# Performance work log

Measured on AMD Instinct MI355X. Metric: run time of the kernel, lower is better.

Reference implementation:

```python
import jax, jax.numpy as jnp
import numpy as np
from jax.ops import segment_sum, segment_max

N, E, B, F, CG = 20000, 320000, 64, 256, 92
NL, NP = 4, 3  # transformer conv layers, ppe layers
SQ = float(np.sqrt(F))


def setup_inputs() -> dict:
    ks = iter(jax.random.split(jax.random.key(0), 64))
    p = lambda *s: jax.random.normal(next(ks), s, jnp.float32) * 0.02
    return {
        "x": jax.random.uniform(next(ks), (N, CG), jnp.float32, 0.0, 10.0),
        "edge_index": jax.random.randint(next(ks), (2, E), 0, N, dtype=jnp.int32),
        "edge_attr": jax.random.normal(next(ks), (E, 3), jnp.float32),
        "batch": jnp.sort(jax.random.randint(next(ks), (N,), 0, B, dtype=jnp.int32)),
        "num_osda": jax.random.uniform(next(ks), (B,), jnp.float32, 1.0, 4.0),
        "ae_W1": p(F, CG), "ae_b1": p(F), "ae_W2": p(F, F), "ae_b2": p(F),
        "ee_W": p(F, F), "ee_b": p(F),
        "pe_W": p(F, CG), "pe_b": p(F),
        "Wq": p(NL, F, F), "bq": p(NL, F), "Wk": p(NL, F, F), "bk": p(NL, F),
        "Wv": p(NL, F, F), "bv": p(NL, F), "We": p(NL, F, F), "be": p(NL, F),
        "Ws": p(NL, F, F), "bs": p(NL, F),
        "pW1": p(NP, 2 * F, F), "pb1": p(NP, 2 * F),
        "pW2": p(NP, F, F), "pb2": p(NP, F),
        "pW3": p(NP, F, F), "pb3": p(NP, F),
        "pg": jnp.ones((NP, F), jnp.float32), "pbeta": jnp.zeros((NP, F), jnp.float32),
        "fc_W": p(F, F), "fc_b": p(F), "out_W": p(1, F), "out_b": p(1),
    }


def _forward(x, edge_index, edge_attr, batch, num_osda, ae_W1, ae_b1, ae_W2, ae_b2,
             ee_W, ee_b, pe_W, pe_b, Wq, bq, Wk, bk, Wv, bv, We, be, Ws, bs,
             pW1, pb1, pW2, pb2, pW3, pb3, pg, pbeta, fc_W, fc_b, out_W, out_b):
    src, dst = edge_index[0], edge_index[1]
    # atom embedding on floor(x): Lin -> SiLU -> Lin
    h = jax.nn.silu(jnp.floor(x) @ ae_W1.T + ae_b1) @ ae_W2.T + ae_b2   # [N,F]
    # ppe embedding on frac(x)*1000
    ppe = ((x - jnp.trunc(x)) * 1000.0) @ pe_W.T + pe_b                 # [N,F]
    # edge embedding: scalar -1/||edge_attr|| -> RBF(vmin=-6,vmax=0,bins=256) -> Lin -> SiLU
    d = -1.0 / jnp.linalg.norm(edge_attr, axis=1)                       # [E]
    centers = jnp.linspace(-6.0, 0.0, F)
    gamma = 1.0 / (6.0 / (F - 1))  # 1/mean(diff(centers))
    rbf = jnp.exp(-gamma * (d[:, None] - centers) ** 2)                 # [E,F]
    ef = jax.nn.silu(rbf @ ee_W.T + ee_b)                               # [E,F]

    def conv(h, i):
        # graph transformer conv (heads=1): softmax over incoming edges per node
        q = h @ Wq[i].T + bq[i]
        k = h @ Wk[i].T + bk[i]
        v = h @ Wv[i].T + bv[i]
        e = ef @ We[i].T + be[i]
        kj = k[src] + e                                                 # [E,F]
        vj = v[src] + e                                                 # [E,F]
        s = jnp.sum(q[dst] * kj, axis=-1) / SQ                          # [E]
        m = segment_max(s, dst, num_segments=N)
        ex = jnp.exp(s - m[dst])
        den = segment_sum(ex, dst, num_segments=N)
        alpha = ex / den[dst]
        agg = segment_sum(alpha[:, None] * vj, dst, num_segments=N)     # [N,F]
        return agg + h @ Ws[i].T + bs[i]                                # root/skip

    def ppe_conv(h, adj, i):
        adj = adj + h
        bn = adj * pg[i] + pbeta[i]  # eval-mode BatchNorm1d (running mean 0, var 1)
        a2 = bn @ pW1[i].T + pb1[i]                                     # [N,2F]
        x1 = a2[:, :F] @ pW2[i].T + pb2[i]
        x2 = jax.nn.gelu(a2[:, F:], approximate=False)  # dropout = identity (eval)
        return (x1 * x2) @ pW3[i].T + pb3[i] + h, adj

    for i in range(NP):
        h = conv(h, i)
        h, ppe = ppe_conv(h, ppe, i)
    h = conv(h, NL - 1)

    # scatter-mean pooling over graphs
    cnt = jnp.maximum(segment_sum(jnp.ones((N,), h.dtype), batch, num_segments=B), 1.0)
    tot = segment_sum(h, batch, num_segments=B) / cnt[:, None]          # [B,F]
    crystal = tot + jax.nn.silu(tot @ fc_W.T + fc_b)
    out = crystal @ out_W.T + out_b                                     # [B,1]
    return jnp.squeeze(out, -1) / num_osda                             # [B]


def reference(x, edge_index, edge_attr, batch, num_osda, ae_W1, ae_b1, ae_W2, ae_b2,
              ee_W, ee_b, pe_W, pe_b, Wq, bq, Wk, bk, Wv, bv, We, be, Ws, bs,
              pW1, pb1, pW2, pb2, pW3, pb3, pg, pbeta, fc_W, fc_b, out_W, out_b):
    return _forward(x, edge_index, edge_attr, batch, num_osda, ae_W1, ae_b1, ae_W2, ae_b2,
                    ee_W, ee_b, pe_W, pe_b, Wq, bq, Wk, bk, Wv, bv, We, be, Ws, bs,
                    pW1, pb1, pW2, pb2, pW3, pb3, pg, pbeta, fc_W, fc_b, out_W, out_b)
```

## Files before the change

### kernel.cpp

```cpp
#include <hip/hip_runtime.h>
#include <cstdint>
#include <cstddef>


#define DEVFN static __device__ __forceinline__

DEVFN float siluf(float x) { return x / (1.f + expf(-x)); }

DEVFN unsigned short f2bf(float x) {
    union { float f; unsigned u; } v; v.f = x;
    return (unsigned short)((v.u + 0x7FFFu + ((v.u >> 16) & 1u)) >> 16);
}
DEVFN float bf2f(unsigned short h) {
    union { unsigned u; float f; } v; v.u = ((unsigned)h) << 16;
    return v.f;
}

typedef __attribute__((ext_vector_type(8))) short bf16x8;
typedef __attribute__((ext_vector_type(4))) float f32x4;

template <int ACT>
__launch_bounds__(256) __global__
void gemm_sw(const float* __restrict__ A, int lda,
             const short* __restrict__ Whi, const short* __restrict__ Wlo, int Kp,
             const float* __restrict__ bias,
             const float* __restrict__ res, int ldr,
             float* __restrict__ C, int ldc,
             int M, int K, int OUT)
{
    constexpr int LDP = 40;
    __shared__ short AsH[128 * LDP];
    __shared__ short AsL[128 * LDP];
    __shared__ short WsH[128 * LDP];
    __shared__ short WsL[128 * LDP];
    const int tid = threadIdx.x;
    const int bm = blockIdx.x * 128;
    const int bn = blockIdx.y * 128;
    const int w = tid >> 6, lane = tid & 63;
    const int wm = (w >> 1) * 64, wn = (w & 1) * 64;
    const int lr = lane & 15, lc = lane >> 4;

    f32x4 acc[4][4];
#pragma unroll
    for (int i = 0; i < 4; ++i)
#pragma unroll
        for (int j = 0; j < 4; ++j) acc[i][j] = (f32x4){0.f, 0.f, 0.f, 0.f};

    const int srow = tid & 127;
    const int scol0 = (tid >> 7) * 16;

    for (int k0 = 0; k0 < K; k0 += 32) {
        {
            int gm = bm + srow;
            const float* ap = A + (size_t)gm * lda + k0 + scol0;
            short sh[16], sl[16];
#pragma unroll
            for (int q = 0; q < 4; ++q) {
                int c = k0 + scol0 + q * 4;
                float4 vv = {0.f, 0.f, 0.f, 0.f};
                if (gm < M) {
                    if (c + 3 < K) {
                        vv = *reinterpret_cast<const float4*>(ap + q * 4);
                    } else {
                        if (c < K)     vv.x = ap[q * 4 + 0];
                        if (c + 1 < K) vv.y = ap[q * 4 + 1];
                        if (c + 2 < K) vv.z = ap[q * 4 + 2];
                        if (c + 3 < K) vv.w = ap[q * 4 + 3];
                    }
                }
                float e[4] = {vv.x, vv.y, vv.z, vv.w};
#pragma unroll
                for (int t = 0; t < 4; ++t) {
                    unsigned short hi = f2bf(e[t]);
                    sh[q * 4 + t] = (short)hi;
                    sl[q * 4 + t] = (short)f2bf(e[t] - bf2f(hi));
                }
            }
            *reinterpret_cast<bf16x8*>(&AsH[srow * LDP + scol0])     = *reinterpret_cast<bf16x8*>(&sh[0]);
            *reinterpret_cast<bf16x8*>(&AsH[srow * LDP + scol0 + 8]) = *reinterpret_cast<bf16x8*>(&sh[8]);
            *reinterpret_cast<bf16x8*>(&AsL[srow * LDP + scol0])     = *reinterpret_cast<bf16x8*>(&sl[0]);
            *reinterpret_cast<bf16x8*>(&AsL[srow * LDP + scol0 + 8]) = *reinterpret_cast<bf16x8*>(&sl[8]);
        }
        {
            int go = bn + srow;
            if (go < OUT) {
                const short* wh = Whi + (size_t)go * Kp + k0 + scol0;
                const short* wl = Wlo + (size_t)go * Kp + k0 + scol0;
                *reinterpret_cast<bf16x8*>(&WsH[srow * LDP + scol0])     = *reinterpret_cast<const bf16x8*>(wh);
                *reinterpret_cast<bf16x8*>(&WsH[srow * LDP + scol0 + 8]) = *reinterpret_cast<const bf16x8*>(wh + 8);
                *reinterpret_cast<bf16x8*>(&WsL[srow * LDP + scol0])     = *reinterpret_cast<const bf16x8*>(wl);
                *reinterpret_cast<bf16x8*>(&WsL[srow * LDP + scol0 + 8]) = *reinterpret_cast<const bf16x8*>(wl + 8);
            } else {
                bf16x8 z = {0, 0, 0, 0, 0, 0, 0, 0};
                *reinterpret_cast<bf16x8*>(&WsH[srow * LDP + scol0])     = z;
                *reinterpret_cast<bf16x8*>(&WsH[srow * LDP + scol0 + 8]) = z;
                *reinterpret_cast<bf16x8*>(&WsL[srow * LDP + scol0])     = z;
                *reinterpret_cast<bf16x8*>(&WsL[srow * LDP + scol0 + 8]) = z;
            }
        }
        __syncthreads();

        bf16x8 afh[4], afl[4], bfh[4], bfl[4];
#pragma unroll
        for (int f = 0; f < 4; ++f) {
            afh[f] = *reinterpret_cast<const bf16x8*>(&AsH[(wm + f * 16 + lr) * LDP + lc * 8]);
            afl[f] = *reinterpret_cast<const bf16x8*>(&AsL[(wm + f * 16 + lr) * LDP + lc * 8]);
            bfh[f] = *reinterpret_cast<const bf16x8*>(&WsH[(wn + f * 16 + lr) * LDP + lc * 8]);
            bfl[f] = *reinterpret_cast<const bf16x8*>(&WsL[(wn + f * 16 + lr) * LDP + lc * 8]);
        }
#pragma unroll
        for (int i = 0; i < 4; ++i)
#pragma unroll
            for (int j = 0; j < 4; ++j) {
                acc[i][j] = __builtin_amdgcn_mfma_f32_16x16x32_bf16(afh[i], bfh[j], acc[i][j], 0, 0, 0);
                acc[i][j] = __builtin_amdgcn_mfma_f32_16x16x32_bf16(afh[i], bfl[j], acc[i][j], 0, 0, 0);
                acc[i][j] = __builtin_amdgcn_mfma_f32_16x16x32_bf16(afl[i], bfh[j], acc[i][j], 0, 0, 0);
            }
        __syncthreads();
    }

#pragma unroll
    for (int i = 0; i < 4; ++i) {
#pragma unroll
        for (int j = 0; j < 4; ++j) {
            int col = bn + wn + j * 16 + lr;
            if (col >= OUT) continue;
            float bv = bias ? bias[col] : 0.f;
#pragma unroll
            for (int r = 0; r < 4; ++r) {
                int m = bm + wm + i * 16 + lc * 4 + r;
                if (m < M) {
                    float v = acc[i][j][r] + bv;
                    if (ACT == 1) v = siluf(v);
                    if (res) v += res[(size_t)m * ldr + col];
                    C[(size_t)m * ldc + col] = v;
                }
            }
        }
    }
}

template <int BM, int BN, int TM, int TN, int ACT>
__launch_bounds__(256) __global__
void gemm_nt(const float* __restrict__ A, int lda,
             const float* __restrict__ W,
             const float* __restrict__ bias,
             const float* __restrict__ res, int ldr,
             float* __restrict__ C, int ldc,
             int M, int K, int OUT)
{
    constexpr int BK = 16;
    __shared__ alignas(16) float As[BK][BM];
    __shared__ alignas(16) float Bs[BK][BN];
    const int tid = threadIdx.x;
    const int bm = blockIdx.x * BM;
    const int bn = blockIdx.y * BN;
    const int tr = (tid >> 4) * TM;
    const int tc = (tid & 15) * TN;

    float acc[TM][TN];
#pragma unroll
    for (int i = 0; i < TM; ++i)
#pragma unroll
        for (int j = 0; j < TN; ++j) acc[i][j] = 0.f;

    for (int k0 = 0; k0 < K; k0 += BK) {
#pragma unroll
        for (int it = 0; it < BM / 64; ++it) {
            int idx = tid + it * 256;
            int m = idx >> 2, kq = idx & 3;
            int gm = bm + m, gk = k0 + kq * 4;
            float t[4] = {0.f, 0.f, 0.f, 0.f};
            if (gm < M) {
#pragma unroll
                for (int j = 0; j < 4; ++j)
                    if (gk + j < K) t[j] = A[(size_t)gm * lda + gk + j];
            }
            As[kq * 4 + 0][m] = t[0];
            As[kq * 4 + 1][m] = t[1];
            As[kq * 4 + 2][m] = t[2];
            As[kq * 4 + 3][m] = t[3];
        }
#pragma unroll
        for (int it = 0; it < BN / 64; ++it) {
            int idx = tid + it * 256;
            int o = idx >> 2, kq = idx & 3;
            int go = bn + o, gk = k0 + kq * 4;
            float t[4] = {0.f, 0.f, 0.f, 0.f};
            if (go < OUT) {
#pragma unroll
                for (int j = 0; j < 4; ++j)
                    if (gk + j < K) t[j] = W[(size_t)go * K + gk + j];
            }
            Bs[kq * 4 + 0][o] = t[0];
            Bs[kq * 4 + 1][o] = t[1];
            Bs[kq * 4 + 2][o] = t[2];
            Bs[kq * 4 + 3][o] = t[3];
        }
        __syncthreads();
#pragma unroll
        for (int kk = 0; kk < BK; ++kk) {
            float a[TM], b[TN];
#pragma unroll
            for (int p = 0; p < TM; ++p) a[p] = As[kk][tr + p];
#pragma unroll
            for (int p = 0; p < TN; ++p) b[p] = Bs[kk][tc + p];
#pragma unroll
            for (int i = 0; i < TM; ++i)
#pragma unroll
                for (int j = 0; j < TN; ++j) acc[i][j] += a[i] * b[j];
        }
        __syncthreads();
    }

#pragma unroll
    for (int i = 0; i < TM; ++i) {
        int m = bm + tr + i;
        if (m >= M) continue;
#pragma unroll
        for (int j = 0; j < TN; ++j) {
            int o = bn + tc + j;
            if (o >= OUT) continue;
            float v = acc[i][j];
            if (bias) v += bias[o];
            if (ACT == 1) v = siluf(v);
            if (res) v += res[(size_t)m * ldr + o];
            C[(size_t)m * ldc + o] = v;
        }
    }
}

__global__ void split_w_k(const float* __restrict__ src, short* __restrict__ dhi,
                          short* __restrict__ dlo, int OUT, int K, int Kp)
{
    int idx = blockIdx.x * blockDim.x + threadIdx.x;
    if (idx >= OUT * Kp) return;
    int row = idx / Kp, col = idx - row * Kp;
    float v = (col < K) ? src[(size_t)row * K + col] : 0.f;
    unsigned short hi = f2bf(v);
    dhi[idx] = (short)hi;
    dlo[idx] = (short)f2bf(v - bf2f(hi));
}

__global__ void stack_qkvs_w_k(const float* __restrict__ Wq, const float* __restrict__ Wk,
                               const float* __restrict__ Wv, const float* __restrict__ Ws,
                               short* __restrict__ dhi, short* __restrict__ dlo, int total)
{
    int idx = blockIdx.x * blockDim.x + threadIdx.x;
    if (idx >= total) return;
    int col = idx & 255;
    int row = (idx >> 8) & 1023;
    int layer = idx >> 18;
    int s2 = row >> 8;
    const float* s = (s2 == 0) ? Wq : ((s2 == 1) ? Wk : ((s2 == 2) ? Wv : Ws));
    float v = s[(size_t)layer * 65536 + (size_t)(row & 255) * 256 + col];
    unsigned short hi = f2bf(v);
    dhi[idx] = (short)hi;
    dlo[idx] = (short)f2bf(v - bf2f(hi));
}

__global__ void stack_qkvs_b_k(const float* __restrict__ bq, const float* __restrict__ bk,
                               const float* __restrict__ bv, const float* __restrict__ bs,
                               float* __restrict__ dst, int total)
{
    int idx = blockIdx.x * blockDim.x + threadIdx.x;
    if (idx >= total) return;
    int r = idx & 1023, layer = idx >> 10;
    int s2 = r >> 8;
    const float* s = (s2 == 0) ? bq : ((s2 == 1) ? bk : ((s2 == 2) ? bv : bs));
    dst[idx] = s[layer * 256 + (r & 255)];
}

__global__ void node_prep_k(const float* __restrict__ x, float* __restrict__ fx,
                            float* __restrict__ px, int n)
{
    int i = blockIdx.x * blockDim.x + threadIdx.x;
    if (i < n) {
        float v = x[i];
        fx[i] = floorf(v);
        px[i] = (v - truncf(v)) * 1000.f;
    }
}

__global__ void table_rbf_k(float* __restrict__ out, int T, float dmin, float step)
{
    int idx = blockIdx.x * blockDim.x + threadIdx.x;
    if (idx >= T * 64) return;
    int t = idx >> 6, j4 = (idx & 63) * 4;
    float dv = dmin + step * (float)t;
    float r[4];
#pragma unroll
    for (int j = 0; j < 4; ++j) {
        float c = -6.f + 6.f * (float)(j4 + j) * (1.f / 255.f);
        float u = dv - c;
        r[j] = expf(-42.5f * u * u);
    }
    float4 v = {r[0], r[1], r[2], r[3]};
    *reinterpret_cast<float4*>(out + (size_t)t * 256 + j4) = v;
}

__global__ void edge_prep_k(const float* __restrict__ ea, int* __restrict__ i0,
                            float* __restrict__ fr, int E, float dmin, float invstep, int T)
{
    int i = blockIdx.x * blockDim.x + threadIdx.x;
    if (i < E) {
        float a = ea[(size_t)i * 3], b = ea[(size_t)i * 3 + 1], c = ea[(size_t)i * 3 + 2];
        float d = -1.f / sqrtf(a * a + b * b + c * c);
        float u = (d - dmin) * invstep;
        u = fminf(fmaxf(u, 0.f), (float)(T - 1) - 1e-3f);
        int t0 = (int)u;
        i0[i] = t0;
        fr[i] = u - (float)t0;
    }
}

__global__ void ppe_prep_k(float* __restrict__ ppe, const float* __restrict__ h,
                           const float* __restrict__ pg, const float* __restrict__ pbeta,
                           float* __restrict__ bn, int n)
{
    int i = blockIdx.x * blockDim.x + threadIdx.x;
    if (i < n) {
        float adj = ppe[i] + h[i];
        ppe[i] = adj;
        int f = i & 255;
        bn[i] = adj * pg[f] + pbeta[f];
    }
}

__global__ void gate_k(const float* __restrict__ x1, const float* __restrict__ a2,
                       float* __restrict__ g, int n)
{
    int i = blockIdx.x * blockDim.x + threadIdx.x;
    if (i < n) {
        int m = i >> 8, f = i & 255;
        float x2 = a2[(size_t)m * 512 + 256 + f];
        float ge = 0.5f * x2 * (1.f + erff(x2 * 0.70710678118654752f));
        g[i] = x1[i] * ge;
    }
}

__global__ void hist_k(const int* __restrict__ dst, int* __restrict__ deg, int E)
{
    int i = blockIdx.x * blockDim.x + threadIdx.x;
    if (i < E) atomicAdd(&deg[dst[i]], 1);
}

__global__ void scan_k(const int* __restrict__ deg, int* __restrict__ off, int n)
{
    __shared__ int buf[1024];
    __shared__ int carry;
    const int t = threadIdx.x;
    if (t == 0) carry = 0;
    __syncthreads();
    for (int base = 0; base < n; base += 1024) {
        int i = base + t;
        int v = (i < n) ? deg[i] : 0;
        buf[t] = v;
        __syncthreads();
        for (int s = 1; s < 1024; s <<= 1) {
            int add = (t >= s) ? buf[t - s] : 0;
            __syncthreads();
            buf[t] += add;
            __syncthreads();
        }
        if (i < n) off[i] = carry + buf[t] - v;
        __syncthreads();
        if (t == 0) carry += buf[1023];
        __syncthreads();
    }
    if (t == 0) off[n] = carry;
}

__global__ void copy_int_k(const int* __restrict__ a, int* __restrict__ b, int n)
{
    int i = blockIdx.x * blockDim.x + threadIdx.x;
    if (i < n) b[i] = a[i];
}

__global__ void scatter_k(const int* __restrict__ dst, int* __restrict__ cursor,
                          int* __restrict__ esort, int E)
{
    int i = blockIdx.x * blockDim.x + threadIdx.x;
    if (i < E) {
        int p = atomicAdd(&cursor[dst[i]], 1);
        esort[p] = i;
    }
}

__launch_bounds__(256) __global__
void attn_fused_k(const float* __restrict__ qkvs, const float* __restrict__ etab,
                  const int* __restrict__ ei0, const float* __restrict__ efr,
                  const int* __restrict__ src, const int* __restrict__ esort,
                  const int* __restrict__ off, float* __restrict__ hn, int Nn)
{
    int node = blockIdx.x * 4 + (threadIdx.x >> 6);
    if (node >= Nn) return;
    int lane = threadIdx.x & 63;
    int lo = off[node], hi = off[node + 1];

    const float* qrow = qkvs + (size_t)node * 1024;
    float4 qv = *reinterpret_cast<const float4*>(qrow + lane * 4);
    float4 sk = *reinterpret_cast<const float4*>(qrow + 768 + lane * 4);

    float m = -3.4e38f, den = 0.f;
    float ax = 0.f, ay = 0.f, az = 0.f, aw = 0.f;

    for (int jj = lo; jj < hi; ++jj) {
        int eid = esort[jj];
        int sp = src[eid];
        int t0 = ei0[eid];
        float f = efr[eid];
        const float* srow = qkvs + (size_t)sp * 1024;
        float4 kv = *reinterpret_cast<const float4*>(srow + 256 + lane * 4);
        float4 e0 = *reinterpret_cast<const float4*>(etab + (size_t)t0 * 256 + lane * 4);
        float4 e1 = *reinterpret_cast<const float4*>(etab + (size_t)(t0 + 1) * 256 + lane * 4);
        float ex0 = e0.x + f * (e1.x - e0.x);
        float ex1 = e0.y + f * (e1.y - e0.y);
        float ex2 = e0.z + f * (e1.z - e0.z);
        float ex3 = e0.w + f * (e1.w - e0.w);
        float p = qv.x * (kv.x + ex0) + qv.y * (kv.y + ex1) +
                  qv.z * (kv.z + ex2) + qv.w * (kv.w + ex3);
#pragma unroll
        for (int s = 32; s; s >>= 1) p += __shfl_xor(p, s, 64);
        p *= 0.0625f;
        float4 vv = *reinterpret_cast<const float4*>(srow + 512 + lane * 4);
        float vx0 = vv.x + ex0, vx1 = vv.y + ex1, vx2 = vv.z + ex2, vx3 = vv.w + ex3;
        if (p > m) {
            float sc = expf(m - p);
            den = den * sc + 1.f;
            ax = ax * sc + vx0;
            ay = ay * sc + vx1;
            az = az * sc + vx2;
            aw = aw * sc + vx3;
            m = p;
        } else {
            float wgt = expf(p - m);
            den += wgt;
            ax += wgt * vx0;
            ay += wgt * vx1;
            az += wgt * vx2;
            aw += wgt * vx3;
        }
    }
    float inv = (hi > lo) ? 1.f / den : 0.f;
    float4 o = {sk.x + ax * inv, sk.y + ay * inv, sk.z + az * inv, sk.w + aw * inv};
    *reinterpret_cast<float4*>(hn + (size_t)node * 256 + lane * 4) = o;
}

__launch_bounds__(256) __global__
void pool_mean_k(const float* __restrict__ h, const int* __restrict__ batch,
                 float* __restrict__ tot, int Nn)
{
    int g = blockIdx.x;
    __shared__ int sl, sh;
    if (threadIdx.x == 0) {
        int lo = 0, hi = Nn;
        while (lo < hi) { int mid = (lo + hi) >> 1; if (batch[mid] < g) lo = mid + 1; else hi = mid; }
        sl = lo;
        lo = 0; hi = Nn;
        while (lo < hi) { int mid = (lo + hi) >> 1; if (batch[mid] < g + 1) lo = mid + 1; else hi = mid; }
        sh = lo;
    }
    __syncthreads();
    float acc = 0.f;
    for (int n = sl; n < sh; ++n) acc += h[(size_t)n * 256 + threadIdx.x];
    float c = (float)(sh - sl);
    if (c < 1.f) c = 1.f;
    tot[(size_t)g * 256 + threadIdx.x] = acc / c;
}

__launch_bounds__(256) __global__
void out_k(const float* __restrict__ crystal, const float* __restrict__ oW,
           const float* __restrict__ ob, const float* __restrict__ nosda,
           float* __restrict__ out, int Bn)
{
    int b = blockIdx.x;
    __shared__ float red[256];
    float p = crystal[(size_t)b * 256 + threadIdx.x] * oW[threadIdx.x];
    red[threadIdx.x] = p;
    __syncthreads();
    for (int s = 128; s; s >>= 1) {
        if (threadIdx.x < s) red[threadIdx.x] += red[threadIdx.x + s];
        __syncthreads();
    }
    if (threadIdx.x == 0) out[b] = (red[0] + ob[0]) / nosda[b];
}

extern "C" void kernel_launch(void* const* d_in, const int* in_sizes, int n_in,
                              void* d_out, int out_size, void* d_ws, size_t ws_size,
                              hipStream_t stream)
{
    const float* x     = (const float*)d_in[0];
    const int*   ei    = (const int*)d_in[1];
    const float* ea    = (const float*)d_in[2];
    const int*   batch = (const int*)d_in[3];
    const float* nosda = (const float*)d_in[4];
    const float* ae_W1 = (const float*)d_in[5];
    const float* ae_b1 = (const float*)d_in[6];
    const float* ae_W2 = (const float*)d_in[7];
    const float* ae_b2 = (const float*)d_in[8];
    const float* ee_W  = (const float*)d_in[9];
    const float* ee_b  = (const float*)d_in[10];
    const float* pe_W  = (const float*)d_in[11];
    const float* pe_b  = (const float*)d_in[12];
    const float* Wq    = (const float*)d_in[13];
    const float* bq    = (const float*)d_in[14];
    const float* Wk    = (const float*)d_in[15];
    const float* bk    = (const float*)d_in[16];
    const float* Wv    = (const float*)d_in[17];
    const float* bv    = (const float*)d_in[18];
    const float* We    = (const float*)d_in[19];
    const float* be    = (const float*)d_in[20];
    const float* Ws    = (const float*)d_in[21];
    const float* bs    = (const float*)d_in[22];
    const float* pW1   = (const float*)d_in[23];
    const float* pb1   = (const float*)d_in[24];
    const float* pW2   = (const float*)d_in[25];
    const float* pb2   = (const float*)d_in[26];
    const float* pW3   = (const float*)d_in[27];
    const float* pb3   = (const float*)d_in[28];
    const float* pg    = (const float*)d_in[29];
    const float* pbeta = (const float*)d_in[30];
    const float* fc_W  = (const float*)d_in[31];
    const float* fc_b  = (const float*)d_in[32];
    const float* out_W = (const float*)d_in[33];
    const float* out_b = (const float*)d_in[34];

    const int CG = 92, F = 256;
    const int N = in_sizes[0] / CG;
    const int E = in_sizes[1] / 2;
    const int B = in_sizes[4];
    const int T = 4096;
    const float DMIN = -8.f, DMAX = 0.f;
    const float STEP = (DMAX - DMIN) / (float)(T - 1);
    const int* src  = ei;
    const int* dstp = ei + E;

    float* w = (float*)d_ws;
    auto take = [&](size_t n) { float* p = w; w += n; return p; };
    auto takeS = [&](size_t nshorts) { short* p = (short*)w; w += (nshorts + 1) / 2; return p; };
    const size_t NF = (size_t)N * F;
    const size_t NCG = (size_t)N * CG;
    float* hb0  = take(NF);
    float* hb1  = take(NF);
    float* ppeb = take(NF);
    float* s1   = take(NF);
    float* arena = take((size_t)N * 1024);
    float* qkvs = arena;
    float* a2b  = arena;
    float* s2b  = arena + 2 * NF;
    float* s3   = arena + 3 * NF;
    float* fx   = arena;
    float* px   = arena + NCG;
    float* rbft = arena + 2 * NCG;
    float* eft  = arena + 2 * NCG + (size_t)T * F;
    float* etab = take((size_t)4 * T * F);
    float* efr  = take(E);
    float* totb = take((size_t)B * F);
    float* cryb = take((size_t)B * F);
    float* bstk = take(4 * 1024);
    short* qwHi = takeS((size_t)4 * 1024 * 256);
    short* qwLo = takeS((size_t)4 * 1024 * 256);
    short* eeHi = takeS((size_t)256 * 256);
    short* eeLo = takeS((size_t)256 * 256);
    short* weHi = takeS((size_t)4 * 256 * 256);
    short* weLo = takeS((size_t)4 * 256 * 256);
    short* a1Hi = takeS((size_t)256 * 96);
    short* a1Lo = takeS((size_t)256 * 96);
    short* a2Hi = takeS((size_t)256 * 256);
    short* a2Lo = takeS((size_t)256 * 256);
    short* peHi = takeS((size_t)256 * 96);
    short* peLo = takeS((size_t)256 * 96);
    short* p1Hi = takeS((size_t)3 * 512 * 256);
    short* p1Lo = takeS((size_t)3 * 512 * 256);
    short* p2Hi = takeS((size_t)3 * 256 * 256);
    short* p2Lo = takeS((size_t)3 * 256 * 256);
    short* p3Hi = takeS((size_t)3 * 256 * 256);
    short* p3Lo = takeS((size_t)3 * 256 * 256);
    int* ei0    = (int*)w; w += E;
    int* deg    = (int*)w; w += N;
    int* offb   = (int*)w; w += (N + 1);
    int* curb   = (int*)w; w += N;
    int* esort  = (int*)w; w += E;
    size_t need = (size_t)((char*)w - (char*)d_ws);
    if (need > ws_size) return;
    (void)n_in; (void)out_size;

    dim3 blk(256);
    auto g1 = [](int n) { return dim3((n + 255) / 256); };

    auto gsw = [&](const float* A, int lda, const short* Whi, const short* Wlo, int Kp,
                   const float* bias, const float* res, int ldr, float* C, int ldc,
                   int M, int K, int OUT, int act) {
        dim3 grid((M + 127) / 128, (OUT + 127) / 128);
        if (act)
            gemm_sw<1><<<grid, blk, 0, stream>>>(A, lda, Whi, Wlo, Kp, bias, res, ldr, C, ldc, M, K, OUT);
        else
            gemm_sw<0><<<grid, blk, 0, stream>>>(A, lda, Whi, Wlo, Kp, bias, res, ldr, C, ldc, M, K, OUT);
    };

    node_prep_k<<<g1(N * CG), blk, 0, stream>>>(x, fx, px, N * CG);
    edge_prep_k<<<g1(E), blk, 0, stream>>>(ea, ei0, efr, E, DMIN, 1.f / STEP, T);
    table_rbf_k<<<g1(T * 64), blk, 0, stream>>>(rbft, T, DMIN, STEP);

    stack_qkvs_w_k<<<g1(4 * 1024 * 256), blk, 0, stream>>>(Wq, Wk, Wv, Ws, qwHi, qwLo, 4 * 1024 * 256);
    stack_qkvs_b_k<<<g1(4 * 1024), blk, 0, stream>>>(bq, bk, bv, bs, bstk, 4 * 1024);
    split_w_k<<<g1(256 * 256), blk, 0, stream>>>(ee_W, eeHi, eeLo, 256, 256, 256);
    split_w_k<<<g1(4 * 256 * 256), blk, 0, stream>>>(We, weHi, weLo, 1024, 256, 256);
    split_w_k<<<g1(256 * 96), blk, 0, stream>>>(ae_W1, a1Hi, a1Lo, 256, 92, 96);
    split_w_k<<<g1(256 * 256), blk, 0, stream>>>(ae_W2, a2Hi, a2Lo, 256, 256, 256);
    split_w_k<<<g1(256 * 96), blk, 0, stream>>>(pe_W, peHi, peLo, 256, 92, 96);
    split_w_k<<<g1(3 * 512 * 256), blk, 0, stream>>>(pW1, p1Hi, p1Lo, 1536, 256, 256);
    split_w_k<<<g1(3 * 256 * 256), blk, 0, stream>>>(pW2, p2Hi, p2Lo, 768, 256, 256);
    split_w_k<<<g1(3 * 256 * 256), blk, 0, stream>>>(pW3, p3Hi, p3Lo, 768, 256, 256);

    gsw(rbft, F, eeHi, eeLo, 256, ee_b, nullptr, 0, eft, F, T, F, F, 1);
    for (int i = 0; i < 4; ++i)
        gsw(eft, F, weHi + (size_t)i * 65536, weLo + (size_t)i * 65536, 256,
            be + (size_t)i * F, nullptr, 0, etab + (size_t)i * T * F, F, T, F, F, 0);

    gsw(fx, CG, a1Hi, a1Lo, 96, ae_b1, nullptr, 0, s1, F, N, CG, F, 1);
    gsw(s1, F, a2Hi, a2Lo, 256, ae_b2, nullptr, 0, hb0, F, N, F, F, 0);
    gsw(px, CG, peHi, peLo, 96, pe_b, nullptr, 0, ppeb, F, N, CG, F, 0);

    hipMemsetAsync(deg, 0, (size_t)N * sizeof(int), stream);
    hist_k<<<g1(E), blk, 0, stream>>>(dstp, deg, E);
    scan_k<<<1, 1024, 0, stream>>>(deg, offb, N);
    copy_int_k<<<g1(N), blk, 0, stream>>>(offb, curb, N);
    scatter_k<<<g1(E), blk, 0, stream>>>(dstp, curb, esort, E);

    float* h  = hb0;
    float* hn = hb1;
    for (int i = 0; i < 4; ++i) {
        gsw(h, F, qwHi + (size_t)i * 1024 * 256, qwLo + (size_t)i * 1024 * 256, 256,
            bstk + (size_t)i * 1024, nullptr, 0, qkvs, 1024, N, F, 1024, 0);

        attn_fused_k<<<dim3((N + 3) / 4), blk, 0, stream>>>(
            qkvs, etab + (size_t)i * T * F, ei0, efr, src, esort, offb, hn, N);
        { float* t = h; h = hn; hn = t; }

        if (i < 3) {
            ppe_prep_k<<<g1(N * F), blk, 0, stream>>>(ppeb, h, pg + (size_t)i * F, pbeta + (size_t)i * F, s1, N * F);
            gsw(s1, F, p1Hi + (size_t)i * 512 * 256, p1Lo + (size_t)i * 512 * 256, 256,
                pb1 + (size_t)i * 2 * F, nullptr, 0, a2b, 2 * F, N, F, 2 * F, 0);
            gsw(a2b, 2 * F, p2Hi + (size_t)i * 65536, p2Lo + (size_t)i * 65536, 256,
                pb2 + (size_t)i * F, nullptr, 0, s2b, F, N, F, F, 0);
            gate_k<<<g1(N * F), blk, 0, stream>>>(s2b, a2b, s3, N * F);
            gsw(s3, F, p3Hi + (size_t)i * 65536, p3Lo + (size_t)i * 65536, 256,
                pb3 + (size_t)i * F, h, F, hn, F, N, F, F, 0);
            { float* t = h; h = hn; hn = t; }
        }
    }

    pool_mean_k<<<dim3(B), blk, 0, stream>>>(h, batch, totb, N);
    {
        dim3 grid((B + 63) / 64, (F + 63) / 64);
        gemm_nt<64, 64, 4, 4, 1><<<grid, blk, 0, stream>>>(totb, F, fc_W, fc_b, totb, F, cryb, F, B, F, F);
    }
    out_k<<<dim3(B), blk, 0, stream>>>(cryb, out_W, out_b, nosda, (float*)d_out, B);
}
```

Baseline: 1.834 ms.

## Feed GEMMs pre-split bf16 hi/lo planes produced by upstream kernel epilogues

The split-bf16 GEMM now reads activations that are already stored as bf16 hi/lo planes, instead of loading fp32 and splitting in its inner loop. Producers do the split in their epilogues: elementwise prep kernels, the RBF table, the gate kernel, and GEMMs through new output modes (planes only, fp32 plus planes, and a PPE mode that separates the two halves). The PPE first GEMM also writes its second half contiguously, so the gate kernel reads it without striding. This removes repeated conversion ALU work and the ragged K-edge load paths from every GEMM tile. The cost is extra plane stores in some epilogues and more buffer aliasing in the arena.

```diff
diff --git a/kernel.cpp b/kernel.cpp
--- a/kernel.cpp
+++ b/kernel.cpp
@@ -19,14 +19,19 @@
 typedef __attribute__((ext_vector_type(8))) short bf16x8;
 typedef __attribute__((ext_vector_type(4))) float f32x4;
 
-template <int ACT>
+#define O_F32    0
+#define O_F32P   1
+#define O_PPE1   4
+#define O_PLANES 5
+
+template <int ACT, int OMODE>
 __launch_bounds__(256) __global__
-void gemm_sw(const float* __restrict__ A, int lda,
-             const short* __restrict__ Whi, const short* __restrict__ Wlo, int Kp,
-             const float* __restrict__ bias,
-             const float* __restrict__ res, int ldr,
-             float* __restrict__ C, int ldc,
-             int M, int K, int OUT)
+void gemm_spp(const short* __restrict__ Ahi, const short* __restrict__ Alo, int lda,
+              const short* __restrict__ Whi, const short* __restrict__ Wlo, int ldw,
+              const float* __restrict__ bias,
+              const float* __restrict__ res, int ldr,
+              float* __restrict__ C, short* __restrict__ P1, short* __restrict__ P2,
+              int ldc, int M, int OUT, int K)
 {
     constexpr int LDP = 40;
     __shared__ short AsH[128 * LDP];
@@ -52,40 +57,26 @@
     for (int k0 = 0; k0 < K; k0 += 32) {
         {
             int gm = bm + srow;
-            const float* ap = A + (size_t)gm * lda + k0 + scol0;
-            short sh[16], sl[16];
-#pragma unroll
-            for (int q = 0; q < 4; ++q) {
-                int c = k0 + scol0 + q * 4;
-                float4 vv = {0.f, 0.f, 0.f, 0.f};
-                if (gm < M) {
-                    if (c + 3 < K) {
-                        vv = *reinterpret_cast<const float4*>(ap + q * 4);
-                    } else {
-                        if (c < K)     vv.x = ap[q * 4 + 0];
-                        if (c + 1 < K) vv.y = ap[q * 4 + 1];
-                        if (c + 2 < K) vv.z = ap[q * 4 + 2];
-                        if (c + 3 < K) vv.w = ap[q * 4 + 3];
-                    }
-                }
-                float e[4] = {vv.x, vv.y, vv.z, vv.w};
-#pragma unroll
-                for (int t = 0; t < 4; ++t) {
-                    unsigned short hi = f2bf(e[t]);
-                    sh[q * 4 + t] = (short)hi;
-                    sl[q * 4 + t] = (short)f2bf(e[t] - bf2f(hi));
-                }
-            }
-            *reinterpret_cast<bf16x8*>(&AsH[srow * LDP + scol0])     = *reinterpret_cast<bf16x8*>(&sh[0]);
-            *reinterpret_cast<bf16x8*>(&AsH[srow * LDP + scol0 + 8]) = *reinterpret_cast<bf16x8*>(&sh[8]);
-            *reinterpret_cast<bf16x8*>(&AsL[srow * LDP + scol0])     = *reinterpret_cast<bf16x8*>(&sl[0]);
-            *reinterpret_cast<bf16x8*>(&AsL[srow * LDP + scol0 + 8]) = *reinterpret_cast<bf16x8*>(&sl[8]);
+            if (gm < M) {
+                const short* ah = Ahi + (size_t)gm * lda + k0 + scol0;
+                const short* al = Alo + (size_t)gm * lda + k0 + scol0;
+                *reinterpret_cast<bf16x8*>(&AsH[srow * LDP + scol0])     = *reinterpret_cast<const bf16x8*>(ah);
+                *reinterpret_cast<bf16x8*>(&AsH[srow * LDP + scol0 + 8]) = *reinterpret_cast<const bf16x8*>(ah + 8);
+                *reinterpret_cast<bf16x8*>(&AsL[srow * LDP + scol0])     = *reinterpret_cast<const bf16x8*>(al);
+                *reinterpret_cast<bf16x8*>(&AsL[srow * LDP + scol0 + 8]) = *reinterpret_cast<const bf16x8*>(al + 8);
+            } else {
+                bf16x8 z = {0, 0, 0, 0, 0, 0, 0, 0};
+                *reinterpret_cast<bf16x8*>(&AsH[srow * LDP + scol0])     = z;
+                *reinterpret_cast<bf16x8*>(&AsH[srow * LDP + scol0 + 8]) = z;
+                *reinterpret_cast<bf16x8*>(&AsL[srow * LDP + scol0])     = z;
+                *reinterpret_cast<bf16x8*>(&AsL[srow * LDP + scol0 + 8]) = z;
+            }
         }
         {
             int go = bn + srow;
             if (go < OUT) {
-                const short* wh = Whi + (size_t)go * Kp + k0 + scol0;
-                const short* wl = Wlo + (size_t)go * Kp + k0 + scol0;
+                const short* wh = Whi + (size_t)go * ldw + k0 + scol0;
+                const short* wl = Wlo + (size_t)go * ldw + k0 + scol0;
                 *reinterpret_cast<bf16x8*>(&WsH[srow * LDP + scol0])     = *reinterpret_cast<const bf16x8*>(wh);
                 *reinterpret_cast<bf16x8*>(&WsH[srow * LDP + scol0 + 8]) = *reinterpret_cast<const bf16x8*>(wh + 8);
                 *reinterpret_cast<bf16x8*>(&WsL[srow * LDP + scol0])     = *reinterpret_cast<const bf16x8*>(wl);
@@ -129,11 +120,30 @@
 #pragma unroll
             for (int r = 0; r < 4; ++r) {
                 int m = bm + wm + i * 16 + lc * 4 + r;
-                if (m < M) {
-                    float v = acc[i][j][r] + bv;
-                    if (ACT == 1) v = siluf(v);
+                if (m >= M) continue;
+                float v = acc[i][j][r] + bv;
+                if (ACT == 1) v = siluf(v);
+                if (OMODE == O_F32) {
                     if (res) v += res[(size_t)m * ldr + col];
                     C[(size_t)m * ldc + col] = v;
+                } else if (OMODE == O_F32P) {
+                    if (res) v += res[(size_t)m * ldr + col];
+                    C[(size_t)m * ldc + col] = v;
+                    unsigned short hi = f2bf(v);
+                    P1[(size_t)m * ldc + col] = (short)hi;
+                    P2[(size_t)m * ldc + col] = (short)f2bf(v - bf2f(hi));
+                } else if (OMODE == O_PPE1) {
+                    if (col < 256) {
+                        unsigned short hi = f2bf(v);
+                        P1[(size_t)m * 256 + col] = (short)hi;
+                        P2[(size_t)m * 256 + col] = (short)f2bf(v - bf2f(hi));
+                    } else {
+                        C[(size_t)m * 256 + (col - 256)] = v;
+                    }
+                } else {
+                    unsigned short hi = f2bf(v);
+                    P1[(size_t)m * ldc + col] = (short)hi;
+                    P2[(size_t)m * ldc + col] = (short)f2bf(v - bf2f(hi));
                 }
             }
         }
@@ -271,32 +281,44 @@
     dst[idx] = s[layer * 256 + (r & 255)];
 }
 
-__global__ void node_prep_k(const float* __restrict__ x, float* __restrict__ fx,
-                            float* __restrict__ px, int n)
-{
-    int i = blockIdx.x * blockDim.x + threadIdx.x;
-    if (i < n) {
-        float v = x[i];
-        fx[i] = floorf(v);
-        px[i] = (v - truncf(v)) * 1000.f;
-    }
-}
-
-__global__ void table_rbf_k(float* __restrict__ out, int T, float dmin, float step)
+__global__ void node_prep_k(const float* __restrict__ x,
+                            short* __restrict__ fxHi, short* __restrict__ fxLo,
+                            short* __restrict__ pxHi, short* __restrict__ pxLo, int n96)
+{
+    int idx = blockIdx.x * blockDim.x + threadIdx.x;
+    if (idx >= n96) return;
+    int n = idx / 96, c = idx - n * 96;
+    float fv = 0.f, pv = 0.f;
+    if (c < 92) {
+        float v = x[(size_t)n * 92 + c];
+        fv = floorf(v);
+        pv = (v - truncf(v)) * 1000.f;
+    }
+    unsigned short h1 = f2bf(fv);
+    fxHi[idx] = (short)h1; fxLo[idx] = (short)f2bf(fv - bf2f(h1));
+    unsigned short h2 = f2bf(pv);
+    pxHi[idx] = (short)h2; pxLo[idx] = (short)f2bf(pv - bf2f(h2));
+}
+
+__global__ void table_rbf_k(short* __restrict__ dhi, short* __restrict__ dlo,
+                            int T, float dmin, float step)
 {
     int idx = blockIdx.x * blockDim.x + threadIdx.x;
     if (idx >= T * 64) return;
     int t = idx >> 6, j4 = (idx & 63) * 4;
     float dv = dmin + step * (float)t;
-    float r[4];
+    short h4[4], l4[4];
 #pragma unroll
     for (int j = 0; j < 4; ++j) {
         float c = -6.f + 6.f * (float)(j4 + j) * (1.f / 255.f);
         float u = dv - c;
-        r[j] = expf(-42.5f * u * u);
-    }
-    float4 v = {r[0], r[1], r[2], r[3]};
-    *reinterpret_cast<float4*>(out + (size_t)t * 256 + j4) = v;
+        float r = expf(-42.5f * u * u);
+        unsigned short hi = f2bf(r);
+        h4[j] = (short)hi;
+        l4[j] = (short)f2bf(r - bf2f(hi));
+    }
+    *reinterpret_cast<short4*>(dhi + (size_t)t * 256 + j4) = *reinterpret_cast<short4*>(h4);
+    *reinterpret_cast<short4*>(dlo + (size_t)t * 256 + j4) = *reinterpret_cast<short4*>(l4);
 }
 
 __global__ void edge_prep_k(const float* __restrict__ ea, int* __restrict__ i0,
@@ -316,26 +338,31 @@
 
 __global__ void ppe_prep_k(float* __restrict__ ppe, const float* __restrict__ h,
                            const float* __restrict__ pg, const float* __restrict__ pbeta,
-                           float* __restrict__ bn, int n)
+                           short* __restrict__ s1Hi, short* __restrict__ s1Lo, int n)
 {
     int i = blockIdx.x * blockDim.x + threadIdx.x;
     if (i < n) {
         float adj = ppe[i] + h[i];
         ppe[i] = adj;
         int f = i & 255;
-        bn[i] = adj * pg[f] + pbeta[f];
-    }
-}
-
-__global__ void gate_k(const float* __restrict__ x1, const float* __restrict__ a2,
-                       float* __restrict__ g, int n)
+        float bn = adj * pg[f] + pbeta[f];
+        unsigned short hi = f2bf(bn);
+        s1Hi[i] = (short)hi;
+        s1Lo[i] = (short)f2bf(bn - bf2f(hi));
+    }
+}
+
+__global__ void gate_k(const float* __restrict__ x1, const float* __restrict__ x2b,
+                       short* __restrict__ s3Hi, short* __restrict__ s3Lo, int n)
 {
     int i = blockIdx.x * blockDim.x + threadIdx.x;
     if (i < n) {
-        int m = i >> 8, f = i & 255;
-        float x2 = a2[(size_t)m * 512 + 256 + f];
+        float x2 = x2b[i];
         float ge = 0.5f * x2 * (1.f + erff(x2 * 0.70710678118654752f));
-        g[i] = x1[i] * ge;
+        float g = x1[i] * ge;
+        unsigned short hi = f2bf(g);
+        s3Hi[i] = (short)hi;
+        s3Lo[i] = (short)f2bf(g - bf2f(hi));
     }
 }
 
@@ -540,21 +567,15 @@
     auto take = [&](size_t n) { float* p = w; w += n; return p; };
     auto takeS = [&](size_t nshorts) { short* p = (short*)w; w += (nshorts + 1) / 2; return p; };
     const size_t NF = (size_t)N * F;
-    const size_t NCG = (size_t)N * CG;
     float* hb0  = take(NF);
     float* hb1  = take(NF);
     float* ppeb = take(NF);
-    float* s1   = take(NF);
+    short* hHi  = takeS(NF);
+    short* hLo  = takeS(NF);
+    short* s1Hi = takeS(NF);
+    short* s1Lo = takeS(NF);
+    float* etab = take((size_t)4 * T * F);
     float* arena = take((size_t)N * 1024);
-    float* qkvs = arena;
-    float* a2b  = arena;
-    float* s2b  = arena + 2 * NF;
-    float* s3   = arena + 3 * NF;
-    float* fx   = arena;
-    float* px   = arena + NCG;
-    float* rbft = arena + 2 * NCG;
-    float* eft  = arena + 2 * NCG + (size_t)T * F;
-    float* etab = take((size_t)4 * T * F);
     float* efr  = take(E);
     float* totb = take((size_t)B * F);
     float* cryb = take((size_t)B * F);
@@ -586,22 +607,30 @@
     if (need > ws_size) return;
     (void)n_in; (void)out_size;
 
+    short* fxHi = (short*)arena;
+    short* fxLo = fxHi + (size_t)N * 96;
+    short* pxHi = fxLo + (size_t)N * 96;
+    short* pxLo = pxHi + (size_t)N * 96;
+    short* rbHi = pxLo + (size_t)N * 96;
+    short* rbLo = rbHi + (size_t)T * 256;
+    short* efHi = rbLo + (size_t)T * 256;
+    short* efLo = efHi + (size_t)T * 256;
+    short* embHi = efLo + (size_t)T * 256;
+    short* embLo = embHi + NF;
+    float* qkvs = arena;
+    short* a2b1Hi = (short*)arena;
+    short* a2b1Lo = a2b1Hi + NF;
+    float* x2b = arena + NF;
+    float* s2b = x2b + NF;
+    short* s3Hi = (short*)(s2b + NF);
+    short* s3Lo = s3Hi + NF;
+
     dim3 blk(256);
     auto g1 = [](int n) { return dim3((n + 255) / 256); };
 
-    auto gsw = [&](const float* A, int lda, const short* Whi, const short* Wlo, int Kp,
-                   const float* bias, const float* res, int ldr, float* C, int ldc,
-                   int M, int K, int OUT, int act) {
-        dim3 grid((M + 127) / 128, (OUT + 127) / 128);
-        if (act)
-            gemm_sw<1><<<grid, blk, 0, stream>>>(A, lda, Whi, Wlo, Kp, bias, res, ldr, C, ldc, M, K, OUT);
-        else
-            gemm_sw<0><<<grid, blk, 0, stream>>>(A, lda, Whi, Wlo, Kp, bias, res, ldr, C, ldc, M, K, OUT);
-    };
-
-    node_prep_k<<<g1(N * CG), blk, 0, stream>>>(x, fx, px, N * CG);
+    node_prep_k<<<g1(N * 96), blk, 0, stream>>>(x, fxHi, fxLo, pxHi, pxLo, N * 96);
     edge_prep_k<<<g1(E), blk, 0, stream>>>(ea, ei0, efr, E, DMIN, 1.f / STEP, T);
-    table_rbf_k<<<g1(T * 64), blk, 0, stream>>>(rbft, T, DMIN, STEP);
+    table_rbf_k<<<g1(T * 64), blk, 0, stream>>>(rbHi, rbLo, T, DMIN, STEP);
 
     stack_qkvs_w_k<<<g1(4 * 1024 * 256), blk, 0, stream>>>(Wq, Wk, Wv, Ws, qwHi, qwLo, 4 * 1024 * 256);
     stack_qkvs_b_k<<<g1(4 * 1024), blk, 0, stream>>>(bq, bk, bv, bs, bstk, 4 * 1024);
@@ -614,14 +643,25 @@
     split_w_k<<<g1(3 * 256 * 256), blk, 0, stream>>>(pW2, p2Hi, p2Lo, 768, 256, 256);
     split_w_k<<<g1(3 * 256 * 256), blk, 0, stream>>>(pW3, p3Hi, p3Lo, 768, 256, 256);
 
-    gsw(rbft, F, eeHi, eeLo, 256, ee_b, nullptr, 0, eft, F, T, F, F, 1);
-    for (int i = 0; i < 4; ++i)
-        gsw(eft, F, weHi + (size_t)i * 65536, weLo + (size_t)i * 65536, 256,
-            be + (size_t)i * F, nullptr, 0, etab + (size_t)i * T * F, F, T, F, F, 0);
-
-    gsw(fx, CG, a1Hi, a1Lo, 96, ae_b1, nullptr, 0, s1, F, N, CG, F, 1);
-    gsw(s1, F, a2Hi, a2Lo, 256, ae_b2, nullptr, 0, hb0, F, N, F, F, 0);
-    gsw(px, CG, peHi, peLo, 96, pe_b, nullptr, 0, ppeb, F, N, CG, F, 0);
+    {
+        dim3 grid((T + 127) / 128, 2);
+        gemm_spp<1, O_PLANES><<<grid, blk, 0, stream>>>(rbHi, rbLo, 256, eeHi, eeLo, 256,
+                                                        ee_b, nullptr, 0, nullptr, efHi, efLo, 256, T, 256, 256);
+        for (int i = 0; i < 4; ++i)
+            gemm_spp<0, O_F32><<<grid, blk, 0, stream>>>(efHi, efLo, 256,
+                weHi + (size_t)i * 65536, weLo + (size_t)i * 65536, 256,
+                be + (size_t)i * F, nullptr, 0, etab + (size_t)i * T * F, nullptr, nullptr, 256, T, 256, 256);
+    }
+
+    {
+        dim3 grid((N + 127) / 128, 2);
+        gemm_spp<1, O_PLANES><<<grid, blk, 0, stream>>>(fxHi, fxLo, 96, a1Hi, a1Lo, 96,
+                                                        ae_b1, nullptr, 0, nullptr, embHi, embLo, 256, N, 256, 96);
+        gemm_spp<0, O_F32P><<<grid, blk, 0, stream>>>(embHi, embLo, 256, a2Hi, a2Lo, 256,
+                                                      ae_b2, nullptr, 0, hb0, hHi, hLo, 256, N, 256, 256);
+        gemm_spp<0, O_F32><<<grid, blk, 0, stream>>>(pxHi, pxLo, 96, peHi, peLo, 96,
+                                                     pe_b, nullptr, 0, ppeb, nullptr, nullptr, 256, N, 256, 96);
+    }
 
     hipMemsetAsync(deg, 0, (size_t)N * sizeof(int), stream);
     hist_k<<<g1(E), blk, 0, stream>>>(dstp, deg, E);
@@ -632,22 +672,39 @@
     float* h  = hb0;
     float* hn = hb1;
     for (int i = 0; i < 4; ++i) {
-        gsw(h, F, qwHi + (size_t)i * 1024 * 256, qwLo + (size_t)i * 1024 * 256, 256,
-            bstk + (size_t)i * 1024, nullptr, 0, qkvs, 1024, N, F, 1024, 0);
+        {
+            dim3 grid((N + 127) / 128, 8);
+            gemm_spp<0, O_F32><<<grid, blk, 0, stream>>>(hHi, hLo, 256,
+                qwHi + (size_t)i * 262144, qwLo + (size_t)i * 262144, 256,
+                bstk + (size_t)i * 1024, nullptr, 0, qkvs, nullptr, nullptr, 1024, N, 1024, 256);
+        }
 
         attn_fused_k<<<dim3((N + 3) / 4), blk, 0, stream>>>(
             qkvs, etab + (size_t)i * T * F, ei0, efr, src, esort, offb, hn, N);
         { float* t = h; h = hn; hn = t; }
 
         if (i < 3) {
-            ppe_prep_k<<<g1(N * F), blk, 0, stream>>>(ppeb, h, pg + (size_t)i * F, pbeta + (size_t)i * F, s1, N * F);
-            gsw(s1, F, p1Hi + (size_t)i * 512 * 256, p1Lo + (size_t)i * 512 * 256, 256,
-                pb1 + (size_t)i * 2 * F, nullptr, 0, a2b, 2 * F, N, F, 2 * F, 0);
-            gsw(a2b, 2 * F, p2Hi + (size_t)i * 65536, p2Lo + (size_t)i * 65536, 256,
-                pb2 + (size_t)i * F, nullptr, 0, s2b, F, N, F, F, 0);
-            gate_k<<<g1(N * F), blk, 0, stream>>>(s2b, a2b, s3, N * F);
-            gsw(s3, F, p3Hi + (size_t)i * 65536, p3Lo + (size_t)i * 65536, 256,
-                pb3 + (size_t)i * F, h, F, hn, F, N, F, F, 0);
+            ppe_prep_k<<<g1(N * F), blk, 0, stream>>>(ppeb, h, pg + (size_t)i * F, pbeta + (size_t)i * F,
+                                                      s1Hi, s1Lo, N * F);
+            {
+                dim3 grid((N + 127) / 128, 4);
+                gemm_spp<0, O_PPE1><<<grid, blk, 0, stream>>>(s1Hi, s1Lo, 256,
+                    p1Hi + (size_t)i * 131072, p1Lo + (size_t)i * 131072, 256,
+                    pb1 + (size_t)i * 512, nullptr, 0, x2b, a2b1Hi, a2b1Lo, 0, N, 512, 256);
+            }
+            {
+                dim3 grid((N + 127) / 128, 2);
+                gemm_spp<0, O_F32><<<grid, blk, 0, stream>>>(a2b1Hi, a2b1Lo, 256,
+                    p2Hi + (size_t)i * 65536, p2Lo + (size_t)i * 65536, 256,
+                    pb2 + (size_t)i * F, nullptr, 0, s2b, nullptr, nullptr, 256, N, 256, 256);
+            }
+            gate_k<<<g1(N * F), blk, 0, stream>>>(s2b, x2b, s3Hi, s3Lo, N * F);
+            {
+                dim3 grid((N + 127) / 128, 2);
+                gemm_spp<0, O_F32P><<<grid, blk, 0, stream>>>(s3Hi, s3Lo, 256,
+                    p3Hi + (size_t)i * 65536, p3Lo + (size_t)i * 65536, 256,
+                    pb3 + (size_t)i * F, h, 256, hn, hHi, hLo, 256, N, 256, 256);
+            }
             { float* t = h; h = hn; hn = t; }
         }
     }
```

After: 1.858 ms. Within noise of the previous version (+1.3%).
